# Performance work log

Measured on AMD Instinct MI355X. Metric: run time of the kernel, lower is better.

Reference implementation:

```python
import jax, jax.numpy as jnp
import numpy as np

G = 4096   # num_genes
P = 4096   # num_perts
H = 64     # hidden_size
B = 4      # num_graphs
E1 = 81920 # coexpress edges
E2 = 81920 # GO edges
FF = 512   # transformer ffn
NH = 2     # attention heads
INTER, LAT = 32, 16  # VAE dims

def _bn(x, g, b, eps=1e-5):
    # BatchNorm1d in training mode: batch stats (biased var)
    m = x.mean(0); v = x.var(0)
    return (x - m) / jnp.sqrt(v + eps) * g + b

def _ln(x, g, b, eps=1e-5):
    m = x.mean(-1, keepdims=True); v = x.var(-1, keepdims=True)
    return (x - m) / jnp.sqrt(v + eps) * g + b

def _mlp2(x, w1, b1, g1, be1, w2, b2, g2, be2):
    # MLP([a,b,c]) builds Linear->BN->ReLU->Linear->BN (trailing ReLU stripped)
    h = jax.nn.relu(_bn(x @ w1.T + b1, g1, be1))
    return _bn(h @ w2.T + b2, g2, be2)

def _sgconv(x, ei, ew, w, b, n):
    # SGConv K=1: gcn_norm (self loops, symmetric norm) then linear
    src = jnp.concatenate([ei[0], jnp.arange(n)])
    dst = jnp.concatenate([ei[1], jnp.arange(n)])
    wgt = jnp.concatenate([ew, jnp.ones((n,), ew.dtype)])
    deg = jax.ops.segment_sum(wgt, dst, num_segments=n)
    dinv = jnp.where(deg > 0, 1.0 / jnp.sqrt(jnp.where(deg > 0, deg, 1.0)), 0.0)
    norm = dinv[dst] * wgt * dinv[src]
    agg = jax.ops.segment_sum(norm[:, None] * x[src], dst, num_segments=n)
    return agg @ w.T + b

def setup_inputs():
    ks = iter(jax.random.split(jax.random.key(0), 80))
    def nrm(shape, s=0.05):
        return jax.random.normal(next(ks), shape, dtype=jnp.float32) * s
    d = {}
    d['x'] = jax.random.uniform(next(ks), (B * G,), dtype=jnp.float32)
    d['pert_idx'] = jax.random.randint(next(ks), (B, 2), 0, P)
    d['mask'] = jnp.zeros((G, G), jnp.float32)
    d['ei_co'] = jax.random.randint(next(ks), (2, E1), 0, G)
    d['w_co'] = jax.random.uniform(next(ks), (E1,), dtype=jnp.float32)
    d['ei_go'] = jax.random.randint(next(ks), (2, E2), 0, P)
    d['w_go'] = jax.random.uniform(next(ks), (E2,), dtype=jnp.float32)
    d['gene_emb'] = nrm((G, H)); d['emb_pos'] = nrm((G, H)); d['pert_tbl'] = nrm((P, H))
    d['sg_co_w'] = nrm((H, H)); d['sg_co_b'] = jnp.zeros((H,))
    d['sg_go_w'] = nrm((H, H)); d['sg_go_b'] = jnp.zeros((H,))
    d['bn_emb_g'] = jnp.ones((H,)); d['bn_emb_b'] = jnp.zeros((H,))
    for pre, din, dout in [('etv2_1', H, H), ('etv2_2', H, H), ('pf_1', H, H), ('pf_2', H, H), ('rw_1', H, 2 * H), ('rw_2', 2 * H, H)]:
        d[pre + '_w'] = nrm((dout, din)); d[pre + '_b'] = jnp.zeros((dout,))
        d[pre + '_g'] = jnp.ones((dout,)); d[pre + '_be'] = jnp.zeros((dout,))
    d['bnpb_g'] = jnp.ones((H,)); d['bnpb_b'] = jnp.zeros((H,))
    d['attn_in_w'] = nrm((3 * H, H)); d['attn_in_b'] = jnp.zeros((3 * H,))
    d['attn_out_w'] = nrm((H, H)); d['attn_out_b'] = jnp.zeros((H,))
    d['ln1_g'] = jnp.ones((H,)); d['ln1_b'] = jnp.zeros((H,))
    d['ff1_w'] = nrm((FF, H)); d['ff1_b'] = jnp.zeros((FF,))
    d['ff2_w'] = nrm((H, FF)); d['ff2_b'] = jnp.zeros((H,))
    d['ln2_g'] = jnp.ones((H,)); d['ln2_b'] = jnp.zeros((H,))
    d['indv_w1'] = nrm((G, H)); d['indv_b1'] = jnp.zeros((G,))
    d['vae_e1_w'] = nrm((INTER, G)); d['vae_e1_b'] = jnp.zeros((INTER,))
    d['vae_mu_w'] = nrm((LAT, INTER)); d['vae_mu_b'] = jnp.zeros((LAT,))
    d['vae_lv_w'] = nrm((LAT, INTER)); d['vae_lv_b'] = jnp.zeros((LAT,))
    d['vae_d1_w'] = nrm((INTER, LAT)); d['vae_d1_b'] = jnp.zeros((INTER,))
    d['vae_d2_w'] = nrm((G, INTER)); d['vae_d2_b'] = jnp.zeros((G,))
    d['eps'] = jax.random.normal(next(ks), (B, LAT), dtype=jnp.float32)
    return d

def reference(x, pert_idx, mask, ei_co, w_co, ei_go, w_go, gene_emb, emb_pos, pert_tbl, sg_co_w, sg_co_b, sg_go_w, sg_go_b, bn_emb_g, bn_emb_b, etv2_1_w, etv2_1_b, etv2_1_g, etv2_1_be, etv2_2_w, etv2_2_b, etv2_2_g, etv2_2_be, pf_1_w, pf_1_b, pf_1_g, pf_1_be, pf_2_w, pf_2_b, pf_2_g, pf_2_be, rw_1_w, rw_1_b, rw_1_g, rw_1_be, rw_2_w, rw_2_b, rw_2_g, rw_2_be, bnpb_g, bnpb_b, attn_in_w, attn_in_b, attn_out_w, attn_out_b, ln1_g, ln1_b, ff1_w, ff1_b, ff2_w, ff2_b, ln2_g, ln2_b, indv_w1, indv_b1, vae_e1_w, vae_e1_b, vae_mu_w, vae_mu_b, vae_lv_w, vae_lv_b, vae_d1_w, vae_d1_b, vae_d2_w, vae_d2_b, eps):
    # gene base embedding (identical across graphs until pert fusion)
    base = jax.nn.relu(_bn(gene_emb, bn_emb_g, bn_emb_b))               # [G,H]
    pos = _sgconv(emb_pos, ei_co, w_co, sg_co_w, sg_co_b, G)            # 1 gene-GNN layer
    base = base + 0.2 * pos
    base = _mlp2(base, etv2_1_w, etv2_1_b, etv2_1_g, etv2_1_be, etv2_2_w, etv2_2_b, etv2_2_g, etv2_2_be)
    # pert embeddings propagated on GO graph
    pge = _sgconv(pert_tbl, ei_go, w_go, sg_go_w, sg_go_b, P)           # [P,H]
    # per-graph pert_track: sum of pert embeddings (all pert_idx valid)
    psum = pge[pert_idx].sum(axis=1)                                    # [B,H]
    etot = _mlp2(psum, pf_1_w, pf_1_b, pf_1_g, pf_1_be, pf_2_w, pf_2_b, pf_2_g, pf_2_be)
    base_b = base[None, :, :] + etot[:, None, :]                        # [B,G,H]
    flat = jax.nn.relu(_bn(base_b.reshape(B * G, H), bnpb_g, bnpb_b))
    out = _mlp2(flat, rw_1_w, rw_1_b, rw_1_g, rw_1_be, rw_2_w, rw_2_b, rw_2_g, rw_2_be)
    out = out.reshape(B, G, H)
    # transformer encoder layer (post-norm, relu, nhead=2), eval/no-dropout
    qkv = out @ attn_in_w.T + attn_in_b
    q, k, v = jnp.split(qkv, 3, axis=-1)
    hd = H // NH
    q = q.reshape(B, G, NH, hd); k = k.reshape(B, G, NH, hd); v = v.reshape(B, G, NH, hd)
    sc = jnp.einsum('bqhd,bkhd->bhqk', q, k) / np.float32(np.sqrt(hd)) + mask
    a = jax.nn.softmax(sc, axis=-1)
    ctx = jnp.einsum('bhqk,bkhd->bqhd', a, v).reshape(B, G, H)
    att = ctx @ attn_out_w.T + attn_out_b
    h1 = _ln(out + att, ln1_g, ln1_b)
    ff = jax.nn.relu(h1 @ ff1_w.T + ff1_b) @ ff2_w.T + ff2_b
    enc = _ln(h1 + ff, ln2_g, ln2_b)
    # per-gene linear: (enc.unsqueeze(-1)*indv_w1).sum(2)+indv_b1
    pred0 = jnp.einsum('bgh,gh->bg', enc, indv_w1) + indv_b1
    # VAE branch on raw expression
    xr = x.reshape(B, G)
    he = jax.nn.relu(xr @ vae_e1_w.T + vae_e1_b)
    mu = he @ vae_mu_w.T + vae_mu_b
    lv = he @ vae_lv_w.T + vae_lv_b
    z = mu + eps * jnp.exp(0.5 * lv)
    hdc = jax.nn.relu(z @ vae_d1_w.T + vae_d1_b)
    recon = hdc @ vae_d2_w.T + vae_d2_b
    kl = -0.5 * jnp.mean(jnp.sum(1.0 + lv - mu ** 2 - jnp.exp(lv), axis=1))
    recon = jnp.where(xr == 0, 0.0, recon)
    pred = pred0 + recon
    return (pred, kl)
```

## Files before the change

### kernel.cpp

```cpp
#include <hip/hip_runtime.h>
#include <hip/hip_bf16.h>
#include <math.h>

#define GG 4096
#define PP 4096
#define HH 64
#define BB 4
#define E1N 81920
#define E2N 81920
#define FFD 512
#define BNEPS 1e-5f
#define LOG2E 1.44269504088896341f
#define QPRE (0.17677669529663687f * LOG2E)

typedef unsigned short ushort_t;
typedef unsigned int uint_t;
using sh8 = __attribute__((ext_vector_type(8))) short;
using sh4 = __attribute__((ext_vector_type(4))) short;
using f4  = __attribute__((ext_vector_type(4))) float;

#if __has_builtin(__builtin_amdgcn_mfma_f32_16x16x16bf16_1k)
#define MFMA16(a, b, c) __builtin_amdgcn_mfma_f32_16x16x16bf16_1k((a), (b), (c), 0, 0, 0)
#elif __has_builtin(__builtin_amdgcn_mfma_f32_16x16x16_bf16)
#define MFMA16(a, b, c) __builtin_amdgcn_mfma_f32_16x16x16_bf16((a), (b), (c), 0, 0, 0)
#else
static __device__ inline f4 mfma16_asm(sh4 a, sh4 b, f4 c) {
    f4 d;
    asm volatile("v_mfma_f32_16x16x16_bf16 %0, %1, %2, %3"
                 : "=v"(d) : "v"(a), "v"(b), "v"(c));
    return d;
}
#define MFMA16(a, b, c) mfma16_asm((a), (b), (c))
#endif

#define OF_STATS   0
#define OF_DEGCO   2048
#define OF_DEGGO   6144
#define OF_PSLOT   10240
#define OF_ETOT    10752
#define OF_HDC     11008
#define OF_HE      11136
#define OF_AGGCO   12288
#define OF_BASEIN  274432
#define OF_Y1      536576
#define OF_Y2      798720
#define OF_FLAT    1060864
#define OF_RW1     2109440
#define OF_RW2     4206592
#define OF_OUT     5255168
#define OF_QKV     6303744
#define OF_QB      OF_AGGCO
#define OF_KB      (OF_AGGCO + 524288)
#define OF_VF      OF_FLAT
#define OF_OPA     OF_QKV
#define OF_OPB     OF_OUT
#define OF_LP      OF_RW1
#define OPS        1048576
#define OF_W1B     9449472
#define OF_W2B     9465856

#define AGGBLKS 1024

__device__ inline ushort_t f2b(float f) {
    uint_t u = __builtin_bit_cast(uint_t, f);
    u += 0x7FFFu + ((u >> 16) & 1u);
    return (ushort_t)(u >> 16);
}

__device__ inline void gld16(const void* gptr, void* lptr) {
    __builtin_amdgcn_global_load_lds(
        (const __attribute__((address_space(1))) uint_t*)gptr,
        (__attribute__((address_space(3))) uint_t*)lptr, 16, 0, 0);
}

__device__ void dev_vae_he(int bid, const float* __restrict__ x, const float* __restrict__ W,
                           const float* __restrict__ bias, float* he, float* sh) {
    int b = bid >> 5, i = bid & 31;
    float s = 0.f;
    for (int g = threadIdx.x; g < 4096; g += 256) s += x[b * 4096 + g] * W[i * 4096 + g];
    sh[threadIdx.x] = s;
    __syncthreads();
    for (int o = 128; o > 0; o >>= 1) {
        if (threadIdx.x < o) sh[threadIdx.x] += sh[threadIdx.x + o];
        __syncthreads();
    }
    if (threadIdx.x == 0) he[b * 32 + i] = fmaxf(sh[0] + bias[i], 0.f);
}

__device__ void dev_vae_mid(const float* __restrict__ he,
                            const float* __restrict__ muw, const float* __restrict__ mub,
                            const float* __restrict__ lvw, const float* __restrict__ lvb,
                            const float* __restrict__ d1w, const float* __restrict__ d1b,
                            const float* __restrict__ eps, float* hdc, float* klout, float* zs) {
    int t = threadIdx.x;
    if (t < 64) {
        int b = t >> 4, l = t & 15;
        float mu = mub[l], lv = lvb[l];
        for (int i = 0; i < 32; i++) {
            float hv = he[b * 32 + i];
            mu += hv * muw[l * 32 + i];
            lv += hv * lvw[l * 32 + i];
        }
        zs[t] = mu + eps[t] * expf(0.5f * lv);
        float kterm = 1.f + lv - mu * mu - expf(lv);
        for (int o = 32; o > 0; o >>= 1) kterm += __shfl_xor(kterm, o, 64);
        if (t == 0) klout[0] = -0.5f * kterm * 0.25f;
    }
    __syncthreads();
    if (t < 128) {
        int b = t >> 5, i = t & 31;
        float a = d1b[i];
        for (int l = 0; l < 16; l++) a += zs[b * 16 + l] * d1w[i * 16 + l];
        hdc[t] = fmaxf(a, 0.f);
    }
}

__device__ void dev_edge_deg(int bid, const int* __restrict__ ei, const float* __restrict__ w,
                             float* deg, int E) {
    int e = bid * 256 + threadIdx.x;
    if (e < E) atomicAdd(&deg[ei[E + e]], w[e]);
}

__device__ void dev_cs_part(int bid, const float* __restrict__ X, int N,
                            float* sum, float* sumsq, float* sh) {
    int t = threadIdx.x;
    int col = t & 63, ro = t >> 6;
    int rows = N >> 8;
    int r0 = bid * rows;
    float s = 0.f, q = 0.f;
    for (int r = r0 + ro; r < r0 + rows; r += 4) {
        float v = X[r * 64 + col];
        s += v; q += v * v;
    }
    float* ls = sh; float* lq = sh + 256;
    ls[t] = s; lq[t] = q;
    __syncthreads();
    if (t < 64) {
        for (int j = t + 64; j < 256; j += 64) { s += ls[j]; q += lq[j]; }
        atomicAdd(&sum[t], s);
        atomicAdd(&sumsq[t], q);
    }
}

__device__ void dev_edge_agg(int bid, const int* __restrict__ ei, const float* __restrict__ w,
                             const float* __restrict__ deg, const float* __restrict__ x,
                             float* agg) {
    const int h = threadIdx.x & 63;
    const int wid = bid * 4 + (threadIdx.x >> 6);
    const int nw4 = AGGBLKS * 4 * 4;
    for (int e0 = wid * 4; e0 < E1N; e0 += nw4) {
        int srcs[4], dsts[4];
        float norms[4];
        #pragma unroll
        for (int j = 0; j < 4; j++) {
            int e = e0 + j;
            srcs[j] = ei[e];
            dsts[j] = ei[E1N + e];
            norms[j] = rsqrtf(deg[dsts[j]] + 1.f) * w[e] * rsqrtf(deg[srcs[j]] + 1.f);
        }
        float xv[4];
        #pragma unroll
        for (int j = 0; j < 4; j++) xv[j] = x[srcs[j] * HH + h];
        #pragma unroll
        for (int j = 0; j < 4; j++)
            atomicAdd(&agg[dsts[j] * HH + h], norms[j] * xv[j]);
    }
}

__device__ void dev_pert_edges(int bid, const int* __restrict__ pidx, const int* __restrict__ ei,
                               const float* __restrict__ w, const float* __restrict__ deg,
                               const float* __restrict__ tbl, float* pslot) {
    int e = bid * 256 + threadIdx.x;
    if (e >= E2N) return;
    int dst = ei[E2N + e];
    int src = ei[e];
    for (int s = 0; s < 8; s++) {
        if (pidx[s] == dst) {
            float norm = rsqrtf(deg[dst] + 1.f) * w[e] * rsqrtf(deg[src] + 1.f);
            for (int h = 0; h < 64; h++)
                atomicAdd(&pslot[s * 64 + h], norm * tbl[src * 64 + h]);
        }
    }
}

__device__ void dev_base_combine(int bid, const float* __restrict__ gene_emb,
                                 const float* __restrict__ agg, const float* __restrict__ emb_pos,
                                 const float* __restrict__ deg,
                                 const float* __restrict__ W, const float* __restrict__ bias,
                                 const float* __restrict__ bsum, const float* __restrict__ bsq,
                                 const float* __restrict__ bg, const float* __restrict__ bb,
                                 float* out, float* sh) {
    float* Wt = sh;
    float* a = sh + 4160;
    int t = threadIdx.x;
    for (int i = t; i < 4096; i += 256) Wt[(i & 63) * 65 + (i >> 6)] = W[i];
    int rr = t >> 6, h = t & 63;
    int g = bid * 4 + rr;
    a[rr * 64 + h] = agg[g * 64 + h] + emb_pos[g * 64 + h] / (deg[g] + 1.f);
    __syncthreads();
    float y = bias[h];
    const float* ar = a + rr * 64;
    #pragma unroll 8
    for (int k = 0; k < 64; k++) y += ar[k] * Wt[k * 65 + h];
    const float invN = 1.0f / (float)GG;
    float m = bsum[h] * invN;
    float is_ = rsqrtf(bsq[h] * invN - m * m + BNEPS);
    float v = gene_emb[g * 64 + h];
    v = (v - m) * is_ * bg[h] + bb[h];
    v = fmaxf(v, 0.f);
    out[g * 64 + h] = v + 0.2f * y;
}

__device__ void dev_pert_mlp(const float* __restrict__ pslot, const int* __restrict__ pidx,
                             const float* __restrict__ deg, const float* __restrict__ tbl,
                             const float* __restrict__ gw, const float* __restrict__ gb,
                             const float* __restrict__ w1, const float* __restrict__ b1,
                             const float* __restrict__ g1, const float* __restrict__ be1,
                             const float* __restrict__ w2, const float* __restrict__ b2,
                             const float* __restrict__ g2, const float* __restrict__ be2,
                             float* etot, float* sh) {
    float* pge = sh;
    float* psum = sh + 512;
    float* y = sh + 768;
    float* mh = sh + 1024;
    float* ih = sh + 1088;
    int t = threadIdx.x;
    for (int j = t; j < 512; j += 256) {
        int s = j >> 6, h = j & 63;
        int n = pidx[s];
        float invd = 1.0f / (deg[n] + 1.f);
        float acc = gb[h];
        for (int k = 0; k < 64; k++)
            acc += (pslot[s * 64 + k] + tbl[n * 64 + k] * invd) * gw[h * 64 + k];
        pge[j] = acc;
    }
    __syncthreads();
    { int b = t >> 6, h = t & 63; psum[t] = pge[2 * b * 64 + h] + pge[(2 * b + 1) * 64 + h]; }
    __syncthreads();
    { int h = t & 63; int b = t >> 6;
      float acc = b1[h];
      for (int k = 0; k < 64; k++) acc += psum[b * 64 + k] * w1[h * 64 + k];
      y[t] = acc; }
    __syncthreads();
    if (t < 64) {
        float s = 0.f, sq = 0.f;
        for (int b = 0; b < 4; b++) { float v = y[b * 64 + t]; s += v; sq += v * v; }
        float m = s * 0.25f;
        mh[t] = m; ih[t] = rsqrtf(sq * 0.25f - m * m + BNEPS);
    }
    __syncthreads();
    { int h = t & 63;
      float v = (y[t] - mh[h]) * ih[h] * g1[h] + be1[h];
      psum[t] = fmaxf(v, 0.f); }
    __syncthreads();
    { int h = t & 63; int b = t >> 6;
      float acc = b2[h];
      for (int k = 0; k < 64; k++) acc += psum[b * 64 + k] * w2[h * 64 + k];
      y[t] = acc; }
    __syncthreads();
    if (t < 64) {
        float s = 0.f, sq = 0.f;
        for (int b = 0; b < 4; b++) { float v = y[b * 64 + t]; s += v; sq += v * v; }
        float m = s * 0.25f;
        mh[t] = m; ih[t] = rsqrtf(sq * 0.25f - m * m + BNEPS);
    }
    __syncthreads();
    { int h = t & 63;
      etot[t] = (y[t] - mh[h]) * ih[h] * g2[h] + be2[h]; }
}

__global__ void k_fat12(float* ws, const int* __restrict__ ei_co, const float* __restrict__ w_co,
                        const int* __restrict__ ei_go, const float* __restrict__ w_go,
                        const float* __restrict__ gene_emb, const float* __restrict__ x,
                        const float* __restrict__ ve1_w, const float* __restrict__ ve1_b,
                        const float* __restrict__ ff1_w, const float* __restrict__ ff2_w) {
    __shared__ float sh[512];
    int bid = blockIdx.x;
    if (bid < 320) dev_edge_deg(bid, ei_co, w_co, ws + OF_DEGCO, E1N);
    else if (bid < 640) dev_edge_deg(bid - 320, ei_go, w_go, ws + OF_DEGGO, E2N);
    else if (bid < 896) dev_cs_part(bid - 640, gene_emb, GG, ws + OF_STATS, ws + OF_STATS + 128, sh);
    else if (bid < 1024) dev_vae_he(bid - 896, x, ve1_w, ve1_b, ws + OF_HE, sh);
    else {
        int i = (bid - 1024) * 256 + threadIdx.x;
        ushort_t* W1b = (ushort_t*)(ws + OF_W1B);
        ushort_t* W2b = (ushort_t*)(ws + OF_W2B);
        if (i < 32768) W1b[i] = f2b(ff1_w[i]);
        else W2b[i - 32768] = f2b(ff2_w[i - 32768]);
    }
}

__global__ void k_fat3(float* ws, const int* __restrict__ ei_co, const float* __restrict__ w_co,
                       const float* __restrict__ emb_pos, const int* __restrict__ pidx,
                       const int* __restrict__ ei_go, const float* __restrict__ w_go,
                       const float* __restrict__ pert_tbl,
                       const float* __restrict__ vmu_w, const float* __restrict__ vmu_b,
                       const float* __restrict__ vlv_w, const float* __restrict__ vlv_b,
                       const float* __restrict__ vd1_w, const float* __restrict__ vd1_b,
                       const float* __restrict__ veps, float* klout) {
    __shared__ float sh[512];
    int bid = blockIdx.x;
    if (bid < AGGBLKS) dev_edge_agg(bid, ei_co, w_co, ws + OF_DEGCO, emb_pos, ws + OF_AGGCO);
    else if (bid < AGGBLKS + 320)
        dev_pert_edges(bid - AGGBLKS, pidx, ei_go, w_go, ws + OF_DEGGO, pert_tbl, ws + OF_PSLOT);
    else dev_vae_mid(ws + OF_HE, vmu_w, vmu_b, vlv_w, vlv_b, vd1_w, vd1_b, veps,
                     ws + OF_HDC, klout, sh);
}

__global__ void k_fat4(float* ws, const float* __restrict__ gene_emb,
                       const float* __restrict__ emb_pos,
                       const float* __restrict__ sg_co_w, const float* __restrict__ sg_co_b,
                       const float* __restrict__ bn_emb_g, const float* __restrict__ bn_emb_b,
                       const int* __restrict__ pidx, const float* __restrict__ pert_tbl,
                       const float* __restrict__ gw, const float* __restrict__ gb,
                       const float* __restrict__ w1, const float* __restrict__ b1,
                       const float* __restrict__ g1, const float* __restrict__ be1,
                       const float* __restrict__ w2, const float* __restrict__ b2,
                       const float* __restrict__ g2, const float* __restrict__ be2) {
    __shared__ float sh[4416];
    int bid = blockIdx.x;
    if (bid < 1024)
        dev_base_combine(bid, gene_emb, ws + OF_AGGCO, emb_pos, ws + OF_DEGCO,
                         sg_co_w, sg_co_b, ws + OF_STATS, ws + OF_STATS + 128,
                         bn_emb_g, bn_emb_b, ws + OF_BASEIN, sh);
    else
        dev_pert_mlp(ws + OF_PSLOT, pidx, ws + OF_DEGGO, pert_tbl, gw, gb,
                     w1, b1, g1, be1, w2, b2, g2, be2, ws + OF_ETOT, sh);
}

__launch_bounds__(256)
__global__ void k_gemm64(const float* __restrict__ X, const float* __restrict__ W,
                         const float* __restrict__ bias, float* __restrict__ Y,
                         int Cin, int Cout,
                         const float* __restrict__ bnsum, const float* __restrict__ bnsq,
                         const float* __restrict__ bng, const float* __restrict__ bnb,
                         float invN, int relu_in,
                         float* __restrict__ outsum, float* __restrict__ outsq) {
    __shared__ float Xs[64][66];
    __shared__ float Ws[64][66];
    __shared__ float bsc[64], bsh[64];
    const int t = threadIdx.x;
    const int row0 = blockIdx.x * 64, cb = blockIdx.y * 64;
    const int tx = t & 15, ty = t >> 4;
    const int c0 = tx * 4, r0 = ty * 4;
    float acc[4][4];
    #pragma unroll
    for (int j = 0; j < 4; j++)
        #pragma unroll
        for (int i = 0; i < 4; i++) acc[j][i] = 0.f;

    for (int k0 = 0; k0 < Cin; k0 += 64) {
        __syncthreads();
        if (t < 64) {
            float sc = 1.f, sh = 0.f;
            if (bnsum) {
                int c = k0 + t;
                float m = bnsum[c] * invN;
                float is_ = rsqrtf(bnsq[c] * invN - m * m + BNEPS);
                sc = is_ * bng[c]; sh = bnb[c] - m * sc;
            }
            bsc[t] = sc; bsh[t] = sh;
        }
        __syncthreads();
        for (int i = t; i < 1024; i += 256) {
            int r = i >> 4, kq = (i & 15) * 4;
            float4 v = *(const float4*)&X[(size_t)(row0 + r) * Cin + k0 + kq];
            float e0 = v.x * bsc[kq] + bsh[kq];
            float e1 = v.y * bsc[kq + 1] + bsh[kq + 1];
            float e2 = v.z * bsc[kq + 2] + bsh[kq + 2];
            float e3 = v.w * bsc[kq + 3] + bsh[kq + 3];
            if (relu_in) {
                e0 = fmaxf(e0, 0.f); e1 = fmaxf(e1, 0.f);
                e2 = fmaxf(e2, 0.f); e3 = fmaxf(e3, 0.f);
            }
            Xs[r][kq] = e0; Xs[r][kq + 1] = e1; Xs[r][kq + 2] = e2; Xs[r][kq + 3] = e3;
            float4 wv = *(const float4*)&W[(size_t)(cb + r) * Cin + k0 + kq];
            Ws[r][kq] = wv.x; Ws[r][kq + 1] = wv.y; Ws[r][kq + 2] = wv.z; Ws[r][kq + 3] = wv.w;
        }
        __syncthreads();
        #pragma unroll 4
        for (int k = 0; k < 64; k += 2) {
            float2 a[4], b[4];
            #pragma unroll
            for (int j = 0; j < 4; j++) a[j] = *(const float2*)&Xs[r0 + j][k];
            #pragma unroll
            for (int i = 0; i < 4; i++) b[i] = *(const float2*)&Ws[c0 + i][k];
            #pragma unroll
            for (int j = 0; j < 4; j++)
                #pragma unroll
                for (int i = 0; i < 4; i++)
                    acc[j][i] += a[j].x * b[i].x + a[j].y * b[i].y;
        }
    }
    float4 bi = *(const float4*)&bias[cb + c0];
    float scol[4] = {0.f, 0.f, 0.f, 0.f}, qcol[4] = {0.f, 0.f, 0.f, 0.f};
    #pragma unroll
    for (int j = 0; j < 4; j++) {
        float4 o;
        o.x = acc[j][0] + bi.x; o.y = acc[j][1] + bi.y;
        o.z = acc[j][2] + bi.z; o.w = acc[j][3] + bi.w;
        *(float4*)&Y[(size_t)(row0 + r0 + j) * Cout + cb + c0] = o;
        scol[0] += o.x; scol[1] += o.y; scol[2] += o.z; scol[3] += o.w;
        qcol[0] += o.x * o.x; qcol[1] += o.y * o.y;
        qcol[2] += o.z * o.z; qcol[3] += o.w * o.w;
    }
    if (outsum) {
        __syncthreads();
        #pragma unroll
        for (int i = 0; i < 4; i++) { Xs[ty][c0 + i] = scol[i]; Ws[ty][c0 + i] = qcol[i]; }
        __syncthreads();
        if (t < 64) {
            float ss = 0.f, qq = 0.f;
            #pragma unroll
            for (int r = 0; r < 16; r++) { ss += Xs[r][t]; qq += Ws[r][t]; }
            atomicAdd(&outsum[cb + t], ss);
            atomicAdd(&outsq[cb + t], qq);
        }
    }
}

__launch_bounds__(256)
__global__ void k_gemm_rw1(const float* __restrict__ y2, const float* __restrict__ etot,
                           const float* __restrict__ s2sum, const float* __restrict__ s2sq,
                           const float* __restrict__ g2e, const float* __restrict__ b2e,
                           const float* __restrict__ g3, const float* __restrict__ b3,
                           const float* __restrict__ W, const float* __restrict__ bias,
                           float* __restrict__ Y,
                           float* __restrict__ osum, float* __restrict__ osq) {
    __shared__ float Xs[64][66];
    __shared__ float Ws[64][66];
    __shared__ float bsc[64], bsh[64];
    const int t = threadIdx.x;
    const int row0 = blockIdx.x * 64, cb = blockIdx.y * 64;
    const int tx = t & 15, ty = t >> 4;
    const int c0 = tx * 4, r0 = ty * 4;
    const int bb = row0 >> 12;
    if (t < 64) {
        const float iG = 1.0f / 4096.f, iNG = 1.0f / 16384.f;
        float S1 = s2sum[t], S2 = s2sq[t];
        float m2 = S1 * iG;
        float is2 = rsqrtf(S2 * iG - m2 * m2 + BNEPS);
        float sc2 = is2 * g2e[t], sh2 = b2e[t] - m2 * sc2;
        float sz = sc2 * S1 + 4096.f * sh2;
        float szz = sc2 * sc2 * S2 + 2.f * sc2 * sh2 * S1 + 4096.f * sh2 * sh2;
        float e0 = etot[t], e1 = etot[64 + t], e2 = etot[128 + t], e3 = etot[192 + t];
        float se = e0 + e1 + e2 + e3;
        float see = e0 * e0 + e1 * e1 + e2 * e2 + e3 * e3;
        float sumF = 4.f * sz + 4096.f * se;
        float sqF = 4.f * szz + 2.f * sz * se + 4096.f * see;
        float m3 = sumF * iNG;
        float is3 = rsqrtf(sqF * iNG - m3 * m3 + BNEPS);
        float eb = etot[bb * 64 + t];
        bsc[t] = sc2 * is3 * g3[t];
        bsh[t] = (sh2 + eb - m3) * is3 * g3[t] + b3[t];
    }
    __syncthreads();
    for (int i = t; i < 1024; i += 256) {
        int r = i >> 4, kq = (i & 15) * 4;
        int g = (row0 + r) & 4095;
        float4 v = *(const float4*)&y2[(size_t)g * 64 + kq];
        Xs[r][kq] = fmaxf(v.x * bsc[kq] + bsh[kq], 0.f);
        Xs[r][kq + 1] = fmaxf(v.y * bsc[kq + 1] + bsh[kq + 1], 0.f);
        Xs[r][kq + 2] = fmaxf(v.z * bsc[kq + 2] + bsh[kq + 2], 0.f);
        Xs[r][kq + 3] = fmaxf(v.w * bsc[kq + 3] + bsh[kq + 3], 0.f);
        float4 wv = *(const float4*)&W[(size_t)(cb + r) * 64 + kq];
        Ws[r][kq] = wv.x; Ws[r][kq + 1] = wv.y; Ws[r][kq + 2] = wv.z; Ws[r][kq + 3] = wv.w;
    }
    __syncthreads();
    float acc[4][4];
    #pragma unroll
    for (int j = 0; j < 4; j++)
        #pragma unroll
        for (int i = 0; i < 4; i++) acc[j][i] = 0.f;
    #pragma unroll 4
    for (int k = 0; k < 64; k += 2) {
        float2 a[4], b[4];
        #pragma unroll
        for (int j = 0; j < 4; j++) a[j] = *(const float2*)&Xs[r0 + j][k];
        #pragma unroll
        for (int i = 0; i < 4; i++) b[i] = *(const float2*)&Ws[c0 + i][k];
        #pragma unroll
        for (int j = 0; j < 4; j++)
            #pragma unroll
            for (int i = 0; i < 4; i++)
                acc[j][i] += a[j].x * b[i].x + a[j].y * b[i].y;
    }
    float4 bi = *(const float4*)&bias[cb + c0];
    float scol[4] = {0.f, 0.f, 0.f, 0.f}, qcol[4] = {0.f, 0.f, 0.f, 0.f};
    #pragma unroll
    for (int j = 0; j < 4; j++) {
        float4 o;
        o.x = acc[j][0] + bi.x; o.y = acc[j][1] + bi.y;
        o.z = acc[j][2] + bi.z; o.w = acc[j][3] + bi.w;
        *(float4*)&Y[(size_t)(row0 + r0 + j) * 128 + cb + c0] = o;
        scol[0] += o.x; scol[1] += o.y; scol[2] += o.z; scol[3] += o.w;
        qcol[0] += o.x * o.x; qcol[1] += o.y * o.y;
        qcol[2] += o.z * o.z; qcol[3] += o.w * o.w;
    }
    __syncthreads();
    #pragma unroll
    for (int i = 0; i < 4; i++) { Xs[ty][c0 + i] = scol[i]; Ws[ty][c0 + i] = qcol[i]; }
    __syncthreads();
    if (t < 64) {
        float ss = 0.f, qq = 0.f;
        #pragma unroll
        for (int r = 0; r < 16; r++) { ss += Xs[r][t]; qq += Ws[r][t]; }
        atomicAdd(&osum[cb + t], ss);
        atomicAdd(&osq[cb + t], qq);
    }
}

__launch_bounds__(256)
__global__ void k_gemm_qkv(const float* __restrict__ X, const float* __restrict__ W,
                           const float* __restrict__ bias,
                           const float* __restrict__ bnsum, const float* __restrict__ bnsq,
                           const float* __restrict__ bng, const float* __restrict__ bnb,
                           ushort_t* __restrict__ Qb, ushort_t* __restrict__ Kb,
                           ushort_t* __restrict__ Vf) {
    __shared__ float Xs[64][66];
    __shared__ float Ws[64][66];
    __shared__ float bsc[64], bsh[64];
    const int t = threadIdx.x;
    const int row0 = blockIdx.x * 64, yb = blockIdx.y, cb = yb * 64;
    const int tx = t & 15, ty = t >> 4;
    const int c0 = tx * 4, r0 = ty * 4;
    const float invN = 1.0f / (float)(BB * GG);
    if (t < 64) {
        float m = bnsum[t] * invN;
        float is_ = rsqrtf(bnsq[t] * invN - m * m + BNEPS);
        float sc = is_ * bng[t];
        bsc[t] = sc; bsh[t] = bnb[t] - m * sc;
    }
    __syncthreads();
    for (int i = t; i < 1024; i += 256) {
        int r = i >> 4, kq = (i & 15) * 4;
        float4 v = *(const float4*)&X[(size_t)(row0 + r) * 64 + kq];
        Xs[r][kq] = v.x * bsc[kq] + bsh[kq];
        Xs[r][kq + 1] = v.y * bsc[kq + 1] + bsh[kq + 1];
        Xs[r][kq + 2] = v.z * bsc[kq + 2] + bsh[kq + 2];
        Xs[r][kq + 3] = v.w * bsc[kq + 3] + bsh[kq + 3];
        float4 wv = *(const float4*)&W[(size_t)(cb + r) * 64 + kq];
        Ws[r][kq] = wv.x; Ws[r][kq + 1] = wv.y; Ws[r][kq + 2] = wv.z; Ws[r][kq + 3] = wv.w;
    }
    __syncthreads();
    float acc[4][4];
    #pragma unroll
    for (int j = 0; j < 4; j++)
        #pragma unroll
        for (int i = 0; i < 4; i++) acc[j][i] = 0.f;
    #pragma unroll 4
    for (int k = 0; k < 64; k += 2) {
        float2 a[4], b[4];
        #pragma unroll
        for (int j = 0; j < 4; j++) a[j] = *(const float2*)&Xs[r0 + j][k];
        #pragma unroll
        for (int i = 0; i < 4; i++) b[i] = *(const float2*)&Ws[c0 + i][k];
        #pragma unroll
        for (int j = 0; j < 4; j++)
            #pragma unroll
            for (int i = 0; i < 4; i++)
                acc[j][i] += a[j].x * b[i].x + a[j].y * b[i].y;
    }
    float4 bi = *(const float4*)&bias[cb + c0];
    const int b2 = row0 >> 12, tile = (row0 & 4095) >> 6;
    if (yb < 2) {
        ushort_t* Dst = (yb == 0) ? Qb : Kb;
        const float sc2 = (yb == 0) ? QPRE : 1.0f;
        const int h = c0 >> 5, d = c0 & 31;
        #pragma unroll
        for (int j = 0; j < 4; j++) {
            union { ushort_t u[4]; uint2 v; } pk;
            pk.u[0] = f2b((acc[j][0] + bi.x) * sc2);
            pk.u[1] = f2b((acc[j][1] + bi.y) * sc2);
            pk.u[2] = f2b((acc[j][2] + bi.z) * sc2);
            pk.u[3] = f2b((acc[j][3] + bi.w) * sc2);
            int g = (row0 & 4095) + r0 + j;
            *(uint2*)&Dst[((size_t)(b2 * 2 + h) * GG + g) * 32 + d] = pk.v;
        }
    } else {
        __syncthreads();
        #pragma unroll
        for (int j = 0; j < 4; j++) {
            Xs[r0 + j][c0] = acc[j][0] + bi.x;
            Xs[r0 + j][c0 + 1] = acc[j][1] + bi.y;
            Xs[r0 + j][c0 + 2] = acc[j][2] + bi.z;
            Xs[r0 + j][c0 + 3] = acc[j][3] + bi.w;
        }
        __syncthreads();
        #pragma unroll
        for (int h = 0; h < 2; h++) {
            union { ushort_t u[8]; uint4 v; } pk;
            #pragma unroll
            for (int j = 0; j < 8; j++) {
                int idx = t * 8 + j;
                int g2 = idx >> 8, L = (idx >> 2) & 63, i = idx & 3;
                int key = (g2 >> 1) * 16 + ((L >> 4) << 2) + i;
                int d = ((g2 & 1) << 4) + (L & 15);
                pk.u[j] = f2b(Xs[key][h * 32 + d]);
            }
            *(uint4*)&Vf[((size_t)((b2 * 2 + h) * 64 + tile)) * 2048 + t * 8] = pk.v;
        }
    }
}

__launch_bounds__(512, 4)
__global__ void k_attn_mfma(const ushort_t* __restrict__ Qb, const ushort_t* __restrict__ Kb,
                            const ushort_t* __restrict__ Vf, const float* __restrict__ mask,
                            float* __restrict__ opA, float* __restrict__ opB,
                            float* __restrict__ Lp) {
    __shared__ ushort_t Kl[2][4][2048];
    __shared__ ushort_t Vl[2][4][2048];
    const int split = blockIdx.y;
    const int bh0 = blockIdx.z * 4;
    const int q0 = blockIdx.x * 64;
    const int kstart = split * (GG / 4), kend = kstart + (GG / 4);
    const int t = threadIdx.x;
    const int lane = t & 63, w = t >> 6;
    const int qg = w >> 1, kh = w & 1;
    const int l15 = lane & 15, quad = lane >> 4;
    const int i2a = kh * 2, i2b = kh * 2 + 1;

    sh8 qf[4];
    #pragma unroll
    for (int bh = 0; bh < 4; bh++)
        qf[bh] = *(const sh8*)&Qb[((size_t)(bh0 + bh) * GG + q0 + qg * 16 + l15) * 32 + quad * 8];
// ... 82 lines not shown
                int ql = qg * 16 + quad * 4 + r;
                Ox[(bh * 64 + ql) * 32 + l15] = O0[bh][r];
                Ox[(bh * 64 + ql) * 32 + l15 + 16] = O1[bh][r];
            }
            if (quad == 0) Lx[bh * 64 + qg * 16 + l15] = ls[bh];
        }
    }
    __syncthreads();
    if (kh == 1) {
        float* op = (split < 3) ? (opA + (size_t)split * OPS) : opB;
        #pragma unroll
        for (int bh = 0; bh < 4; bh++) {
            int gbh = bh0 + bh;
            #pragma unroll
            for (int r = 0; r < 4; r++) {
                int ql = qg * 16 + quad * 4 + r;
                size_t o = ((size_t)gbh * GG + q0 + ql) * 32 + l15;
                op[o] = O0[bh][r] + Ox[(bh * 64 + ql) * 32 + l15];
                op[o + 16] = O1[bh][r] + Ox[(bh * 64 + ql) * 32 + l15 + 16];
            }
            if (quad == 0)
                Lp[split * 32768 + gbh * GG + q0 + qg * 16 + l15] =
                    ls[bh] + Lx[bh * 64 + qg * 16 + l15];
        }
    }
}

__launch_bounds__(256)
__global__ void k_tail(const float* __restrict__ opA, const float* __restrict__ opB,
                       const float* __restrict__ Lp, const float* __restrict__ yrw2,
                       const float* __restrict__ Waout, const float* __restrict__ baout,
                       const float* __restrict__ bsum5, const float* __restrict__ bsq5,
                       const float* __restrict__ bg5, const float* __restrict__ bb5,
                       const float* __restrict__ lg1, const float* __restrict__ lb1,
                       const ushort_t* __restrict__ W1b, const float* __restrict__ b1f,
                       const ushort_t* __restrict__ W2b, const float* __restrict__ b2f,
                       const float* __restrict__ lg2, const float* __restrict__ lb2,
                       const float* __restrict__ indvw, const float* __restrict__ indvb,
                       const float* __restrict__ hdc, const float* __restrict__ d2w,
                       const float* __restrict__ d2b, const float* __restrict__ x,
                       float* __restrict__ outp) {
    __shared__ float Wt[4160];
    __shared__ float Cs[4160];
    __shared__ ushort_t Hb[4096];
    __shared__ ushort_t FT[32768];
    __shared__ ushort_t WS[2][4096];
    const int t = threadIdx.x;
    const int r0b = blockIdx.x * 64;
    const int lane = t & 63, w = t >> 6;
    const int l15 = lane & 15, quad = lane >> 4;

    for (int i = t; i < 4096; i += 256) Wt[(i & 63) * 65 + (i >> 6)] = Waout[i];
    {
        int col = t & 63, rl = t >> 6;
        int hh = col >> 5, d = col & 31;
        for (int jj = 0; jj < 16; jj++) {
            int lrow = rl + jj * 4;
            int row = r0b + lrow;
            int b = row >> 12, q = row & 4095;
            int bhq = (b * 2 + hh) * GG + q;
            size_t oi = (size_t)bhq * 32 + d;
            float num = opA[oi] + opA[OPS + oi] + opA[2 * OPS + oi] + opB[oi];
            float den = Lp[bhq] + Lp[32768 + bhq] + Lp[65536 + bhq] + Lp[98304 + bhq];
            Cs[lrow * 65 + col] = num / den;
        }
    }
    __syncthreads();
    const float invN = 1.0f / (float)(BB * GG);
    float m5 = bsum5[lane] * invN;
    float is5 = rsqrtf(bsq5[lane] * invN - m5 * m5 + BNEPS);
    float h1v[16];
    for (int j = 0; j < 16; j++) {
        int lrow = w * 16 + j;
        int row = r0b + lrow;
        float acc = baout[lane];
        const float* cr = Cs + lrow * 65;
        #pragma unroll 8
        for (int k = 0; k < 64; k++) acc += cr[k] * Wt[k * 65 + lane];
        float ov = (yrw2[(size_t)row * 64 + lane] - m5) * is5 * bg5[lane] + bb5[lane];
        float v = ov + acc;
        float s = v;
        for (int o = 32; o > 0; o >>= 1) s += __shfl_xor(s, o, 64);
        float mean = s * (1.f / 64.f);
        float d = v - mean;
        float sq = d * d;
        for (int o = 32; o > 0; o >>= 1) sq += __shfl_xor(sq, o, 64);
        float inv = rsqrtf(sq * (1.f / 64.f) + BNEPS);
        h1v[j] = d * inv * lg1[lane] + lb1[lane];
    }
    __syncthreads();
    float* h1f = Wt;
    for (int j = 0; j < 16; j++) h1f[(w * 16 + j) * 65 + lane] = h1v[j];
    __syncthreads();
    if (t < 128) {
        int kt = t >> 6, lane6 = t & 63;
        int q2 = (lane6 >> 4) & 3, r15 = lane6 & 15;
        for (int rg = 0; rg < 4; rg++) {
            union { ushort_t u[8]; uint4 v4; } pk;
            #pragma unroll
            for (int j = 0; j < 8; j++)
                pk.u[j] = f2b(h1f[(rg * 16 + r15) * 65 + kt * 32 + q2 * 8 + j]);
            *(uint4*)&Hb[(rg * 2 + kt) * 512 + lane6 * 8] = pk.v4;
        }
    }
    auto stage1 = [&](int buf, int cb8) {
        int cb = cb8 * 64;
        #pragma unroll
        for (int kt = 0; kt < 2; kt++)
            gld16(W1b + (size_t)((cb + w * 16 + l15) * 64 + kt * 32 + quad * 8),
                  &WS[buf][(w * 2 + kt) * 512 + lane * 8]);
    };
    stage1(0, 0);
    for (int cb8 = 0; cb8 < 8; cb8++) {
        const int cur = cb8 & 1;
        __syncthreads();
        if (cb8 + 1 < 8) stage1(cur ^ 1, cb8 + 1);
        sh8 xf0 = *(const sh8*)&Hb[(w * 2 + 0) * 512 + lane * 8];
        sh8 xf1 = *(const sh8*)&Hb[(w * 2 + 1) * 512 + lane * 8];
        const int cb = cb8 * 64;
        #pragma unroll
        for (int c = 0; c < 4; c++) {
            sh8 wf0 = *(const sh8*)&WS[cur][(c * 2 + 0) * 512 + lane * 8];
            sh8 wf1 = *(const sh8*)&WS[cur][(c * 2 + 1) * 512 + lane * 8];
            f4 z = {0.f, 0.f, 0.f, 0.f};
            f4 acc = __builtin_amdgcn_mfma_f32_16x16x32_bf16(wf0, xf0, z, 0, 0, 0);
            acc = __builtin_amdgcn_mfma_f32_16x16x32_bf16(wf1, xf1, acc, 0, 0, 0);
            float4 bv = *(const float4*)&b1f[cb + c * 16 + quad * 4];
            union { ushort_t u[4]; uint2 v2; } pk;
            pk.u[0] = f2b(fmaxf(acc[0] + bv.x, 0.f));
            pk.u[1] = f2b(fmaxf(acc[1] + bv.y, 0.f));
            pk.u[2] = f2b(fmaxf(acc[2] + bv.z, 0.f));
            pk.u[3] = f2b(fmaxf(acc[3] + bv.w, 0.f));
            int kt512 = cb8 * 2 + (c >> 1);
            int quadp = (c & 1) * 2 + (quad >> 1);
            int j0 = (quad & 1) * 4;
            *(uint2*)&FT[((w * 16 + kt512) * 64 + quadp * 16 + l15) * 8 + j0] = pk.v2;
        }
    }
    auto stage2 = [&](int buf, int k0) {
        #pragma unroll
        for (int kt = 0; kt < 2; kt++)
            gld16(W2b + (size_t)((w * 16 + l15) * 512 + k0 + kt * 32 + quad * 8),
                  &WS[buf][(w * 2 + kt) * 512 + lane * 8]);
    };
    stage2(0, 0);
    f4 acc2[4];
    #pragma unroll
    for (int c = 0; c < 4; c++) acc2[c] = f4{0.f, 0.f, 0.f, 0.f};
    for (int k0 = 0; k0 < 512; k0 += 64) {
        const int cur = (k0 >> 6) & 1;
        __syncthreads();
        if (k0 + 64 < 512) stage2(cur ^ 1, k0 + 64);
        const int ktb = k0 >> 5;
        #pragma unroll
        for (int kt = 0; kt < 2; kt++) {
            sh8 xf = *(const sh8*)&FT[((w * 16 + ktb + kt) * 64 + lane) * 8];
            #pragma unroll
            for (int c = 0; c < 4; c++) {
                sh8 wf = *(const sh8*)&WS[cur][(c * 2 + kt) * 512 + lane * 8];
                acc2[c] = __builtin_amdgcn_mfma_f32_16x16x32_bf16(wf, xf, acc2[c], 0, 0, 0);
            }
        }
    }
    const int row = r0b + w * 16 + l15;
    const int b = row >> 12, g = row & 4095;
    float v[4][4];
    float s = 0.f, sq = 0.f;
    #pragma unroll
    for (int c = 0; c < 4; c++) {
        float4 bv = *(const float4*)&b2f[c * 16 + quad * 4];
        #pragma unroll
        for (int i = 0; i < 4; i++) {
            float hv = h1f[(w * 16 + l15) * 65 + c * 16 + quad * 4 + i];
            float bvi = (i == 0) ? bv.x : (i == 1) ? bv.y : (i == 2) ? bv.z : bv.w;
            v[c][i] = hv + acc2[c][i] + bvi;
            s += v[c][i]; sq += v[c][i] * v[c][i];
        }
    }
    s += __shfl_xor(s, 16, 64);  s += __shfl_xor(s, 32, 64);
    sq += __shfl_xor(sq, 16, 64); sq += __shfl_xor(sq, 32, 64);
    float mean = s * (1.f / 64.f);
    float inv = rsqrtf(sq * (1.f / 64.f) - mean * mean + BNEPS);
    float pd = 0.f;
    #pragma unroll
    for (int c = 0; c < 4; c++) {
        float4 lgv = *(const float4*)&lg2[c * 16 + quad * 4];
        float4 lbv = *(const float4*)&lb2[c * 16 + quad * 4];
        float4 iwv = *(const float4*)&indvw[(size_t)g * 64 + c * 16 + quad * 4];
        pd += ((v[c][0] - mean) * inv * lgv.x + lbv.x) * iwv.x;
        pd += ((v[c][1] - mean) * inv * lgv.y + lbv.y) * iwv.y;
        pd += ((v[c][2] - mean) * inv * lgv.z + lbv.z) * iwv.z;
        pd += ((v[c][3] - mean) * inv * lgv.w + lbv.w) * iwv.w;
    }
    float rc = 0.f;
    #pragma unroll
    for (int i = 0; i < 8; i++)
        rc += hdc[b * 32 + quad * 8 + i] * d2w[(size_t)g * 32 + quad * 8 + i];
    pd += __shfl_xor(pd, 16, 64); pd += __shfl_xor(pd, 32, 64);
    rc += __shfl_xor(rc, 16, 64); rc += __shfl_xor(rc, 32, 64);
    if (quad == 0) {
        float recon = rc + d2b[g];
        if (x[row] == 0.f) recon = 0.f;
        outp[row] = pd + indvb[g] + recon;
    }
}

extern "C" void kernel_launch(void* const* d_in, const int* in_sizes, int n_in,
                              void* d_out, int out_size, void* d_ws, size_t ws_size,
                              hipStream_t stream) {
    const float* x        = (const float*)d_in[0];
    const int*   pert_idx = (const int*)  d_in[1];
    const float* mask     = (const float*)d_in[2];
    const int*   ei_co    = (const int*)  d_in[3];
    const float* w_co     = (const float*)d_in[4];
    const int*   ei_go    = (const int*)  d_in[5];
    const float* w_go     = (const float*)d_in[6];
    const float* gene_emb = (const float*)d_in[7];
    const float* emb_pos  = (const float*)d_in[8];
    const float* pert_tbl = (const float*)d_in[9];
    const float* sg_co_w  = (const float*)d_in[10];
    const float* sg_co_b  = (const float*)d_in[11];
    const float* sg_go_w  = (const float*)d_in[12];
    const float* sg_go_b  = (const float*)d_in[13];
    const float* bn_emb_g = (const float*)d_in[14];
    const float* bn_emb_b = (const float*)d_in[15];
    const float* etv1_w   = (const float*)d_in[16];
    const float* etv1_b   = (const float*)d_in[17];
    const float* etv1_g   = (const float*)d_in[18];
    const float* etv1_be  = (const float*)d_in[19];
    const float* etv2_w   = (const float*)d_in[20];
    const float* etv2_b   = (const float*)d_in[21];
    const float* etv2_g   = (const float*)d_in[22];
    const float* etv2_be  = (const float*)d_in[23];
    const float* pf1_w    = (const float*)d_in[24];
    const float* pf1_b    = (const float*)d_in[25];
    const float* pf1_g    = (const float*)d_in[26];
    const float* pf1_be   = (const float*)d_in[27];
    const float* pf2_w    = (const float*)d_in[28];
    const float* pf2_b    = (const float*)d_in[29];
    const float* pf2_g    = (const float*)d_in[30];
    const float* pf2_be   = (const float*)d_in[31];
    const float* rw1_w    = (const float*)d_in[32];
    const float* rw1_b    = (const float*)d_in[33];
    const float* rw1_g    = (const float*)d_in[34];
    const float* rw1_be   = (const float*)d_in[35];
    const float* rw2_w    = (const float*)d_in[36];
    const float* rw2_b    = (const float*)d_in[37];
    const float* rw2_g    = (const float*)d_in[38];
    const float* rw2_be   = (const float*)d_in[39];
    const float* bnpb_g   = (const float*)d_in[40];
    const float* bnpb_b   = (const float*)d_in[41];
    const float* ain_w    = (const float*)d_in[42];
    const float* ain_b    = (const float*)d_in[43];
    const float* aout_w   = (const float*)d_in[44];
    const float* aout_b   = (const float*)d_in[45];
    const float* ln1_g    = (const float*)d_in[46];
    const float* ln1_b    = (const float*)d_in[47];
    const float* ff1_w    = (const float*)d_in[48];
    const float* ff1_b    = (const float*)d_in[49];
    const float* ff2_w    = (const float*)d_in[50];
    const float* ff2_b    = (const float*)d_in[51];
    const float* ln2_g    = (const float*)d_in[52];
    const float* ln2_b    = (const float*)d_in[53];
    const float* indv_w   = (const float*)d_in[54];
    const float* indv_b   = (const float*)d_in[55];
    const float* ve1_w    = (const float*)d_in[56];
    const float* ve1_b    = (const float*)d_in[57];
    const float* vmu_w    = (const float*)d_in[58];
    const float* vmu_b    = (const float*)d_in[59];
    const float* vlv_w    = (const float*)d_in[60];
    const float* vlv_b    = (const float*)d_in[61];
    const float* vd1_w    = (const float*)d_in[62];
    const float* vd1_b    = (const float*)d_in[63];
    const float* vd2_w    = (const float*)d_in[64];
    const float* vd2_b    = (const float*)d_in[65];
    const float* veps     = (const float*)d_in[66];

    float* ws   = (float*)d_ws;
    float* outp = (float*)d_out;

    float* stm1 = ws + OF_STATS + 1 * 256; float* sti1 = stm1 + 128;
    float* stm2 = ws + OF_STATS + 2 * 256; float* sti2 = stm2 + 128;
    float* stm4 = ws + OF_STATS + 4 * 256; float* sti4 = stm4 + 128;
    float* stm5 = ws + OF_STATS + 5 * 256; float* sti5 = stm5 + 128;

    float* basein = ws + OF_BASEIN;
    float* y1     = ws + OF_Y1;
    float* y2     = ws + OF_Y2;
    float* yrw1   = ws + OF_RW1;
    float* yrw2   = ws + OF_RW2;
    float* opA    = ws + OF_OPA;
    float* opB    = ws + OF_OPB;
    float* Lp     = ws + OF_LP;
    ushort_t* Qb  = (ushort_t*)(ws + OF_QB);
    ushort_t* Kb  = (ushort_t*)(ws + OF_KB);
    ushort_t* Vf  = (ushort_t*)(ws + OF_VF);
    ushort_t* W1b = (ushort_t*)(ws + OF_W1B);
    ushort_t* W2b = (ushort_t*)(ws + OF_W2B);

    const int NG = BB * GG;
    const float iG = 1.0f / (float)GG, iNG = 1.0f / (float)NG;

    hipMemsetAsync(ws, 0, 10752 * sizeof(float), stream);
    hipMemsetAsync(ws + OF_AGGCO, 0, (size_t)GG * HH * sizeof(float), stream);

    k_fat12<<<1280, 256, 0, stream>>>(ws, ei_co, w_co, ei_go, w_go, gene_emb,
                                      x, ve1_w, ve1_b, ff1_w, ff2_w);
    k_fat3<<<AGGBLKS + 321, 256, 0, stream>>>(ws, ei_co, w_co, emb_pos, pert_idx,
                                              ei_go, w_go, pert_tbl,
                                              vmu_w, vmu_b, vlv_w, vlv_b, vd1_w, vd1_b,
                                              veps, outp + NG);
    k_fat4<<<1025, 256, 0, stream>>>(ws, gene_emb, emb_pos, sg_co_w, sg_co_b,
                                     bn_emb_g, bn_emb_b, pert_idx, pert_tbl,
                                     sg_go_w, sg_go_b,
                                     pf1_w, pf1_b, pf1_g, pf1_be,
                                     pf2_w, pf2_b, pf2_g, pf2_be);
    k_gemm64<<<dim3(GG / 64, 1), 256, 0, stream>>>(basein, etv1_w, etv1_b, y1, 64, 64,
                                                   nullptr, nullptr, nullptr, nullptr, 0.f, 0,
                                                   stm1, sti1);
    k_gemm64<<<dim3(GG / 64, 1), 256, 0, stream>>>(y1, etv2_w, etv2_b, y2, 64, 64,
                                                   stm1, sti1, etv1_g, etv1_be, iG, 1,
                                                   stm2, sti2);
    k_gemm_rw1<<<dim3(NG / 64, 2), 256, 0, stream>>>(y2, ws + OF_ETOT, stm2, sti2,
                                                     etv2_g, etv2_be, bnpb_g, bnpb_b,
                                                     rw1_w, rw1_b, yrw1, stm4, sti4);
    k_gemm64<<<dim3(NG / 64, 1), 256, 0, stream>>>(yrw1, rw2_w, rw2_b, yrw2, 128, 64,
                                                   stm4, sti4, rw1_g, rw1_be, iNG, 1,
                                                   stm5, sti5);
    k_gemm_qkv<<<dim3(NG / 64, 3), 256, 0, stream>>>(yrw2, ain_w, ain_b,
                                                     stm5, sti5, rw2_g, rw2_be,
                                                     Qb, Kb, Vf);
    k_attn_mfma<<<dim3(GG / 64, 4, 2), 512, 0, stream>>>(Qb, Kb, Vf, mask, opA, opB, Lp);
    k_tail<<<NG / 64, 256, 0, stream>>>(opA, opB, Lp, yrw2, aout_w, aout_b,
                                        stm5, sti5, rw2_g, rw2_be, ln1_g, ln1_b,
                                        W1b, ff1_b, W2b, ff2_b, ln2_g, ln2_b,
                                        indv_w, indv_b, ws + OF_HDC, vd2_w, vd2_b,
                                        x, outp);
}
```

Before: 511.7 us.

## Replace atomic edge aggregation with CSR build and per-node gather

Coexpression edge aggregation no longer does one float atomic per edge per hidden channel. Instead, in-degree counts are recorded, a single-block scan builds CSR offsets, and edges are scattered into per-destination lists. The combine kernel then pulls neighbor embeddings directly. The pert-edge kernel now uses wave ballots to skip waves with no matching destinations and to spread the 64 channels across lanes. This adds a serial scan launch and an extra scatter pass in exchange for far fewer atomics.

```diff
diff --git a/kernel.cpp b/kernel.cpp
--- a/kernel.cpp
+++ b/kernel.cpp
@@ -40,7 +40,11 @@
 #define OF_ETOT    10752
 #define OF_HDC     11008
 #define OF_HE      11136
-#define OF_AGGCO   12288
+#define OF_CNT     12288
+#define OF_OFFS    16384
+#define OF_WOFF    20608
+#define OF_SSRC    24704
+#define OF_SNRM    106624
 #define OF_BASEIN  274432
 #define OF_Y1      536576
 #define OF_Y2      798720
@@ -49,8 +53,8 @@
 #define OF_RW2     4206592
 #define OF_OUT     5255168
 #define OF_QKV     6303744
-#define OF_QB      OF_AGGCO
-#define OF_KB      (OF_AGGCO + 524288)
+#define OF_QB      12288
+#define OF_KB      (OF_QB + 524288)
 #define OF_VF      OF_FLAT
 #define OF_OPA     OF_QKV
 #define OF_OPB     OF_OUT
@@ -58,8 +62,6 @@
 #define OPS        1048576
 #define OF_W1B     9449472
 #define OF_W2B     9465856
-
-#define AGGBLKS 1024
 
 __device__ inline ushort_t f2b(float f) {
     uint_t u = __builtin_bit_cast(uint_t, f);
@@ -116,9 +118,13 @@
 }
 
 __device__ void dev_edge_deg(int bid, const int* __restrict__ ei, const float* __restrict__ w,
-                             float* deg, int E) {
+                             float* deg, int E, int* cnt) {
     int e = bid * 256 + threadIdx.x;
-    if (e < E) atomicAdd(&deg[ei[E + e]], w[e]);
+    if (e < E) {
+        int d = ei[E + e];
+        atomicAdd(&deg[d], w[e]);
+        if (cnt) atomicAdd(&cnt[d], 1);
+    }
 }
 
 __device__ void dev_cs_part(int bid, const float* __restrict__ X, int N,
@@ -142,49 +148,48 @@
     }
 }
 
-__device__ void dev_edge_agg(int bid, const int* __restrict__ ei, const float* __restrict__ w,
-                             const float* __restrict__ deg, const float* __restrict__ x,
-                             float* agg) {
-    const int h = threadIdx.x & 63;
-    const int wid = bid * 4 + (threadIdx.x >> 6);
-    const int nw4 = AGGBLKS * 4 * 4;
-    for (int e0 = wid * 4; e0 < E1N; e0 += nw4) {
-        int srcs[4], dsts[4];
-        float norms[4];
-        #pragma unroll
-        for (int j = 0; j < 4; j++) {
-            int e = e0 + j;
-            srcs[j] = ei[e];
-            dsts[j] = ei[E1N + e];
-            norms[j] = rsqrtf(deg[dsts[j]] + 1.f) * w[e] * rsqrtf(deg[srcs[j]] + 1.f);
-        }
-        float xv[4];
-        #pragma unroll
-        for (int j = 0; j < 4; j++) xv[j] = x[srcs[j] * HH + h];
-        #pragma unroll
-        for (int j = 0; j < 4; j++)
-            atomicAdd(&agg[dsts[j] * HH + h], norms[j] * xv[j]);
-    }
+__device__ void dev_scatter(int bid, const int* __restrict__ ei, const float* __restrict__ w,
+                            const float* __restrict__ deg,
+                            int* woff, int* ssrc, float* snrm) {
+    int e = bid * 256 + threadIdx.x;
+    if (e >= E1N) return;
+    int src = ei[e], dst = ei[E1N + e];
+    float nrm = rsqrtf(deg[dst] + 1.f) * w[e] * rsqrtf(deg[src] + 1.f);
+    int pos = atomicAdd(&woff[dst], 1);
+    ssrc[pos] = src;
+    snrm[pos] = nrm;
 }
 
 __device__ void dev_pert_edges(int bid, const int* __restrict__ pidx, const int* __restrict__ ei,
                                const float* __restrict__ w, const float* __restrict__ deg,
                                const float* __restrict__ tbl, float* pslot) {
     int e = bid * 256 + threadIdx.x;
-    if (e >= E2N) return;
-    int dst = ei[E2N + e];
-    int src = ei[e];
+    int lane = threadIdx.x & 63;
+    bool valid = e < E2N;
+    int dst = valid ? ei[E2N + e] : -1;
+    int hit = 0;
+    #pragma unroll
+    for (int s = 0; s < 8; s++) hit |= (pidx[s] == dst) ? (1 << s) : 0;
+    if (__ballot(hit != 0) == 0) return;
+    int src = valid ? ei[e] : 0;
+    float nrm = 0.f;
+    if (hit) nrm = rsqrtf(deg[dst] + 1.f) * w[e] * rsqrtf(deg[src] + 1.f);
     for (int s = 0; s < 8; s++) {
-        if (pidx[s] == dst) {
-            float norm = rsqrtf(deg[dst] + 1.f) * w[e] * rsqrtf(deg[src] + 1.f);
-            for (int h = 0; h < 64; h++)
-                atomicAdd(&pslot[s * 64 + h], norm * tbl[src * 64 + h]);
+        unsigned long long m = __ballot((hit >> s) & 1);
+        while (m) {
+            int l = __builtin_ctzll(m);
+            m &= m - 1;
+            int es = __shfl(src, l, 64);
+            float en = __shfl(nrm, l, 64);
+            atomicAdd(&pslot[s * 64 + lane], en * tbl[es * 64 + lane]);
         }
     }
 }
 
 __device__ void dev_base_combine(int bid, const float* __restrict__ gene_emb,
-                                 const float* __restrict__ agg, const float* __restrict__ emb_pos,
+                                 const int* __restrict__ off, const int* __restrict__ ssrc,
+                                 const float* __restrict__ snrm,
+                                 const float* __restrict__ emb_pos,
                                  const float* __restrict__ deg,
                                  const float* __restrict__ W, const float* __restrict__ bias,
                                  const float* __restrict__ bsum, const float* __restrict__ bsq,
@@ -196,7 +201,19 @@
     for (int i = t; i < 4096; i += 256) Wt[(i & 63) * 65 + (i >> 6)] = W[i];
     int rr = t >> 6, h = t & 63;
     int g = bid * 4 + rr;
-    a[rr * 64 + h] = agg[g * 64 + h] + emb_pos[g * 64 + h] / (deg[g] + 1.f);
+    float acc = emb_pos[g * 64 + h] / (deg[g] + 1.f);
+    int e = off[g];
+    const int e1 = off[g + 1];
+    for (; e + 4 <= e1; e += 4) {
+        int s0 = ssrc[e], s1 = ssrc[e + 1], s2 = ssrc[e + 2], s3 = ssrc[e + 3];
+        float n0 = snrm[e], n1 = snrm[e + 1], n2 = snrm[e + 2], n3 = snrm[e + 3];
+        acc += n0 * emb_pos[s0 * 64 + h];
+        acc += n1 * emb_pos[s1 * 64 + h];
+        acc += n2 * emb_pos[s2 * 64 + h];
+        acc += n3 * emb_pos[s3 * 64 + h];
+    }
+    for (; e < e1; e++) acc += snrm[e] * emb_pos[ssrc[e] * 64 + h];
+    a[rr * 64 + h] = acc;
     __syncthreads();
     float y = bias[h];
     const float* ar = a + rr * 64;
@@ -276,8 +293,8 @@
                         const float* __restrict__ ff1_w, const float* __restrict__ ff2_w) {
     __shared__ float sh[512];
     int bid = blockIdx.x;
-    if (bid < 320) dev_edge_deg(bid, ei_co, w_co, ws + OF_DEGCO, E1N);
-    else if (bid < 640) dev_edge_deg(bid - 320, ei_go, w_go, ws + OF_DEGGO, E2N);
+    if (bid < 320) dev_edge_deg(bid, ei_co, w_co, ws + OF_DEGCO, E1N, (int*)(ws + OF_CNT));
+    else if (bid < 640) dev_edge_deg(bid - 320, ei_go, w_go, ws + OF_DEGGO, E2N, nullptr);
     else if (bid < 896) dev_cs_part(bid - 640, gene_emb, GG, ws + OF_STATS, ws + OF_STATS + 128, sh);
     else if (bid < 1024) dev_vae_he(bid - 896, x, ve1_w, ve1_b, ws + OF_HE, sh);
     else {
@@ -289,8 +306,36 @@
     }
 }
 
+__global__ void k_scan(float* ws) {
+    int* cnt = (int*)(ws + OF_CNT);
+    int* off = (int*)(ws + OF_OFFS);
+    int* woff = (int*)(ws + OF_WOFF);
+    __shared__ int part[256];
+    const int t = threadIdx.x;
+    int loc[16];
+    int s = 0;
+    #pragma unroll
+    for (int i = 0; i < 16; i++) { loc[i] = s; s += cnt[t * 16 + i]; }
+    part[t] = s;
+    __syncthreads();
+    for (int o = 1; o < 256; o <<= 1) {
+        int v = (t >= o) ? part[t - o] : 0;
+        __syncthreads();
+        part[t] += v;
+        __syncthreads();
+    }
+    int prev = (t == 0) ? 0 : part[t - 1];
+    #pragma unroll
+    for (int i = 0; i < 16; i++) {
+        int o = prev + loc[i];
+        off[t * 16 + i] = o;
+        woff[t * 16 + i] = o;
+    }
+    if (t == 255) off[4096] = part[255];
+}
+
 __global__ void k_fat3(float* ws, const int* __restrict__ ei_co, const float* __restrict__ w_co,
-                       const float* __restrict__ emb_pos, const int* __restrict__ pidx,
+                       const int* __restrict__ pidx,
                        const int* __restrict__ ei_go, const float* __restrict__ w_go,
                        const float* __restrict__ pert_tbl,
                        const float* __restrict__ vmu_w, const float* __restrict__ vmu_b,
@@ -299,9 +344,11 @@
                        const float* __restrict__ veps, float* klout) {
     __shared__ float sh[512];
     int bid = blockIdx.x;
-    if (bid < AGGBLKS) dev_edge_agg(bid, ei_co, w_co, ws + OF_DEGCO, emb_pos, ws + OF_AGGCO);
-    else if (bid < AGGBLKS + 320)
-        dev_pert_edges(bid - AGGBLKS, pidx, ei_go, w_go, ws + OF_DEGGO, pert_tbl, ws + OF_PSLOT);
+    if (bid < 320)
+        dev_scatter(bid, ei_co, w_co, ws + OF_DEGCO,
+                    (int*)(ws + OF_WOFF), (int*)(ws + OF_SSRC), ws + OF_SNRM);
+    else if (bid < 640)
+        dev_pert_edges(bid - 320, pidx, ei_go, w_go, ws + OF_DEGGO, pert_tbl, ws + OF_PSLOT);
     else dev_vae_mid(ws + OF_HE, vmu_w, vmu_b, vlv_w, vlv_b, vd1_w, vd1_b, veps,
                      ws + OF_HDC, klout, sh);
 }
@@ -319,7 +366,9 @@
     __shared__ float sh[4416];
     int bid = blockIdx.x;
     if (bid < 1024)
-        dev_base_combine(bid, gene_emb, ws + OF_AGGCO, emb_pos, ws + OF_DEGCO,
+        dev_base_combine(bid, gene_emb, (const int*)(ws + OF_OFFS),
+                         (const int*)(ws + OF_SSRC), ws + OF_SNRM,
+                         emb_pos, ws + OF_DEGCO,
                          sg_co_w, sg_co_b, ws + OF_STATS, ws + OF_STATS + 128,
                          bn_emb_g, bn_emb_b, ws + OF_BASEIN, sh);
     else
@@ -1008,14 +1057,15 @@
     const float iG = 1.0f / (float)GG, iNG = 1.0f / (float)NG;
 
     hipMemsetAsync(ws, 0, 10752 * sizeof(float), stream);
-    hipMemsetAsync(ws + OF_AGGCO, 0, (size_t)GG * HH * sizeof(float), stream);
+    hipMemsetAsync(ws + OF_CNT, 0, 4096 * sizeof(int), stream);
 
     k_fat12<<<1280, 256, 0, stream>>>(ws, ei_co, w_co, ei_go, w_go, gene_emb,
                                       x, ve1_w, ve1_b, ff1_w, ff2_w);
-    k_fat3<<<AGGBLKS + 321, 256, 0, stream>>>(ws, ei_co, w_co, emb_pos, pert_idx,
-                                              ei_go, w_go, pert_tbl,
-                                              vmu_w, vmu_b, vlv_w, vlv_b, vd1_w, vd1_b,
-                                              veps, outp + NG);
+    k_scan<<<1, 256, 0, stream>>>(ws);
+    k_fat3<<<641, 256, 0, stream>>>(ws, ei_co, w_co, pert_idx,
+                                    ei_go, w_go, pert_tbl,
+                                    vmu_w, vmu_b, vlv_w, vlv_b, vd1_w, vd1_b,
+                                    veps, outp + NG);
     k_fat4<<<1025, 256, 0, stream>>>(ws, gene_emb, emb_pos, sg_co_w, sg_co_b,
                                      bn_emb_g, bn_emb_b, pert_idx, pert_tbl,
                                      sg_go_w, sg_go_b,
```

Result: faster. 449.7 us (-12.1%).
